# Kernel optimization log

Measured on AMD Instinct MI355X. Metric: run time of the kernel, lower is better.

Reference implementation:

```python
import jax, jax.numpy as jnp
import numpy as np

N_NODES = 65536
N_EDGES = 1048576
D = 128           # input_dim == hidden_dim*heads, residual active everywhere
HEADS = (4, 4, 1) # heads per GATv2 layer; last layer heads=1, out=input_dim
NUM_LAYERS = 3


def setup_inputs() -> dict:
    key = jax.random.key(0)
    ks = jax.random.split(key, 16)
    x = jax.random.normal(ks[0], (N_NODES, D), dtype=jnp.float32)
    edge_src = jax.random.randint(ks[1], (N_EDGES,), 0, N_NODES)
    edge_dst = jax.random.randint(ks[2], (N_EDGES,), 0, N_NODES)
    edge_attr = jax.random.uniform(ks[3], (N_EDGES, 1), dtype=jnp.float32)
    s = 0.05
    Wl = jax.random.normal(ks[4], (NUM_LAYERS, D, D), dtype=jnp.float32) * s
    bl = jnp.zeros((NUM_LAYERS, D), dtype=jnp.float32)
    Wr = jax.random.normal(ks[5], (NUM_LAYERS, D, D), dtype=jnp.float32) * s
    br = jnp.zeros((NUM_LAYERS, D), dtype=jnp.float32)
    We = jax.random.normal(ks[6], (NUM_LAYERS, 1, D), dtype=jnp.float32) * s
    att = jax.random.normal(ks[7], (NUM_LAYERS, D), dtype=jnp.float32) * s  # reshaped (H,C) per layer
    bias_p = jnp.zeros((NUM_LAYERS, D), dtype=jnp.float32)
    ln_g = jnp.ones((NUM_LAYERS, D), dtype=jnp.float32)
    ln_b = jnp.zeros((NUM_LAYERS, D), dtype=jnp.float32)
    return {"x": x, "edge_src": edge_src, "edge_dst": edge_dst, "edge_attr": edge_attr,
            "Wl": Wl, "bl": bl, "Wr": Wr, "br": br, "We": We, "att": att,
            "bias_p": bias_p, "ln_g": ln_g, "ln_b": ln_b, "num_graphs": 128}


def _layer_norm(x, g, b):
    mu = x.mean(-1, keepdims=True)
    var = jnp.mean((x - mu) ** 2, axis=-1, keepdims=True)
    return (x - mu) * jax.lax.rsqrt(var + 1e-5) * g + b


def _gatv2(x, src, dst, ea, Wl, bl, Wr, br, We, att, bias, H):
    # GATv2Conv, eval mode (no dropout), concat heads
    N = x.shape[0]
    HC = Wl.shape[1]
    C = HC // H
    xl = (x @ Wl + bl).reshape(N, H, C)
    xr = (x @ Wr + br).reshape(N, H, C)
    ee = (ea @ We).reshape(-1, H, C)            # [E, H, C]
    m = xl[src] + xr[dst] + ee                  # gather + fuse edge features
    m = jnp.where(m >= 0, m, 0.2 * m)           # leaky_relu(0.2)
    a = jnp.einsum('ehc,hc->eh', m, att.reshape(H, C))
    # scatter-softmax over destination node neighborhoods
    amax = jax.ops.segment_max(a, dst, num_segments=N)
    ae = jnp.exp(a - amax[dst])
    asum = jax.ops.segment_sum(ae, dst, num_segments=N)
    alpha = ae / (asum[dst] + 1e-16)
    out = jax.ops.segment_sum(xl[src] * alpha[:, :, None], dst, num_segments=N)
    return out.reshape(N, HC) + bias


def reference(x, edge_src, edge_dst, edge_attr, Wl, bl, Wr, br, We, att,
              bias_p, ln_g, ln_b, num_graphs):
    N = x.shape[0]
    # add_self_loops=True with fill_value='mean' for edge_attr (PyG default)
    loop = jnp.arange(N, dtype=edge_src.dtype)
    src = jnp.concatenate([edge_src, loop])
    dst = jnp.concatenate([edge_dst, loop])
    ea_mean = edge_attr.mean(0, keepdims=True)
    ea = jnp.concatenate([edge_attr, jnp.broadcast_to(ea_mean, (N, edge_attr.shape[1]))])
    h = x
    for i in range(NUM_LAYERS):
        out = _gatv2(h, src, dst, ea, Wl[i], bl[i], Wr[i], br[i], We[i],
                     att[i], bias_p[i], HEADS[i])
        out = _layer_norm(out, ln_g[i], ln_b[i])
        if i < NUM_LAYERS - 1:
            out = jax.nn.gelu(out, approximate=False)
        h = h + out  # residual: dims match at every layer by construction
    # to_dense_batch with equal-size graphs, then drop virtual node (last per graph)
    x_dense = h.reshape(num_graphs, -1, h.shape[-1])
    return x_dense[:, :-1, :]
```

## Files before the change

### kernel.cpp

```cpp
#include <hip/hip_runtime.h>
#include <hip/hip_bf16.h>

typedef unsigned int uint;
typedef unsigned short ushort;

#define NN 65536
#define NE 1048576
#define DD 128
#define TOTE (NE + NN)

__device__ __forceinline__ float b2f(ushort u) {
    uint v = ((uint)u) << 16; float f; __builtin_memcpy(&f, &v, 4); return f;
}
__device__ __forceinline__ ushort f2b(float f) {
    uint x; __builtin_memcpy(&x, &f, 4);
    uint r = (x + 0x7fffu + ((x >> 16) & 1u)) >> 16;
    return (ushort)r;
}

typedef __bf16 bf16x8 __attribute__((ext_vector_type(8)));
typedef float f32x4 __attribute__((ext_vector_type(4)));
typedef float f32x2 __attribute__((ext_vector_type(2)));

__device__ __forceinline__ f32x2 bf2f2(uint u) {
    union { uint i; float f; } lo, hi;
    lo.i = u << 16; hi.i = u & 0xffff0000u;
    return (f32x2){lo.f, hi.f};
}


__global__ void k_init(const float* __restrict__ Wl, const float* __restrict__ Wr,
                       ushort* __restrict__ WT, int* __restrict__ cnt, float* __restrict__ sumbuf,
                       float* __restrict__ cano) {
    if (cano && blockIdx.x == 0 && blockIdx.y == 0 && blockIdx.z == 0 && threadIdx.x == 0)
        cano[0] = 100.0f;
    int k = blockIdx.x, n = threadIdx.x, lr = blockIdx.y, layer = blockIdx.z;
    const float* W = (lr ? Wr : Wl) + layer * 16384;
    WT[(layer * 2 + lr) * 16384 + n * 128 + k] = f2b(W[k * 128 + n]);
    int gid = ((blockIdx.z * 2 + blockIdx.y) * 128 + blockIdx.x) * 128 + threadIdx.x;
    if (gid < NN) cnt[gid] = 0;
    if (gid == NN) sumbuf[0] = 0.f;
}

__global__ void k_histsum(const int* __restrict__ dst, const float* __restrict__ ea,
                          int* __restrict__ cnt, float* __restrict__ sum,
                          float* __restrict__ cano) {
    if (cano && blockIdx.x == 0 && threadIdx.x == 0) cano[1] = 120.0f;
    __shared__ float red[256];
    int t = threadIdx.x;
    int e0 = (blockIdx.x * 256 + t) * 4;
    float s = 0.f;
    if (e0 < NE) {
        int4  d4 = *(const int4*)&dst[e0];
        float4 a4 = *(const float4*)&ea[e0];
        atomicAdd(&cnt[d4.x], 1); atomicAdd(&cnt[d4.y], 1);
        atomicAdd(&cnt[d4.z], 1); atomicAdd(&cnt[d4.w], 1);
        s = (a4.x + a4.y) + (a4.z + a4.w);
    } else {
        int b = e0 - NE;
        atomicAdd(&cnt[b], 1);     atomicAdd(&cnt[b + 1], 1);
        atomicAdd(&cnt[b + 2], 1); atomicAdd(&cnt[b + 3], 1);
    }
    red[t] = s; __syncthreads();
    for (int o = 128; o > 0; o >>= 1) { if (t < o) red[t] += red[t + o]; __syncthreads(); }
    if (t == 0 && red[0] != 0.f) atomicAdd(sum, red[0]);
}

__global__ void k_scanA(const int* __restrict__ cnt, int* __restrict__ row_off, int* __restrict__ bsum,
                        float* __restrict__ cano) {
    if (cano && blockIdx.x == 0 && threadIdx.x == 0) cano[2] = 140.0f;
    __shared__ int tmp[256];
    int t = threadIdx.x, i = blockIdx.x * 256 + t;
    int v = cnt[i]; tmp[t] = v; __syncthreads();
    for (int off = 1; off < 256; off <<= 1) {
        int x = (t >= off) ? tmp[t - off] : 0;
        __syncthreads();
        tmp[t] += x;
        __syncthreads();
    }
    row_off[i] = tmp[t] - v;
    if (t == 255) bsum[blockIdx.x] = tmp[255];
}

__global__ void k_scanC(int* __restrict__ row_off, const int* __restrict__ bsum, int* __restrict__ cursor,
                        float* __restrict__ cano) {
    if (cano && blockIdx.x == 0 && threadIdx.x == 0) cano[3] = 160.0f;
    __shared__ int tmp[256];
    __shared__ int excl[256];
    int t = threadIdx.x;
    int v = bsum[t]; tmp[t] = v; __syncthreads();
    for (int off = 1; off < 256; off <<= 1) {
        int x = (t >= off) ? tmp[t - off] : 0;
        __syncthreads();
        tmp[t] += x;
        __syncthreads();
    }
    excl[t] = tmp[t] - v;
    __syncthreads();
    int offb = excl[blockIdx.x];
    int i = blockIdx.x * 256 + t;
    int nv = row_off[i] + offb;
    row_off[i] = nv;
    cursor[i] = nv;
    if (i == 0) row_off[NN] = TOTE;
}

__global__ void k_scatter(const int* __restrict__ src, const int* __restrict__ dst,
                          const float* __restrict__ ea, const float* __restrict__ sum,
                          int* __restrict__ cursor, int2* __restrict__ adj,
                          float* __restrict__ cano) {
    if (cano && blockIdx.x == 0 && threadIdx.x == 0) cano[4] = 180.0f;
    int e0 = (blockIdx.x * 256 + threadIdx.x) * 4;
    if (e0 < NE) {
        int4  s4 = *(const int4*)&src[e0];
        int4  d4 = *(const int4*)&dst[e0];
        float4 a4 = *(const float4*)&ea[e0];
        int p0 = atomicAdd(&cursor[d4.x], 1); adj[p0] = make_int2(s4.x << 8, __float_as_int(a4.x));
        int p1 = atomicAdd(&cursor[d4.y], 1); adj[p1] = make_int2(s4.y << 8, __float_as_int(a4.y));
        int p2 = atomicAdd(&cursor[d4.z], 1); adj[p2] = make_int2(s4.z << 8, __float_as_int(a4.z));
        int p3 = atomicAdd(&cursor[d4.w], 1); adj[p3] = make_int2(s4.w << 8, __float_as_int(a4.w));
    } else {
        int b = e0 - NE;
        float a = sum[0] * (1.0f / NE);
        #pragma unroll
        for (int k = 0; k < 4; k++) {
            int p = atomicAdd(&cursor[b + k], 1);
            adj[p] = make_int2((b + k) << 8, __float_as_int(a));
        }
    }
}

template<bool F32SRC>
__global__ __launch_bounds__(512) void k_gemm(const void* __restrict__ srcv, const ushort* __restrict__ WT,
                                              const float* __restrict__ bl, const float* __restrict__ br,
                                              ushort* __restrict__ xl, ushort* __restrict__ xr,
                                              float* __restrict__ cano, int cslot, float cval) {
    if (cano && blockIdx.x == 0 && threadIdx.x == 0) cano[cslot] = cval;
    __shared__ __align__(16) ushort S[32768];

    int t = threadIdx.x;
    int rowbase = blockIdx.x * 128;

    #pragma unroll
    for (int i = 0; i < 8; i++) {
        int idx = i * 512 + t;
        int m = idx >> 11, n = (idx >> 4) & 127, c = idx & 15;
        *(bf16x8*)&S[m * 16384 + c * 1024 + n * 8] =
            *(const bf16x8*)&WT[m * 16384 + n * 128 + c * 8];
    }

    int wave = t >> 6, lane = t & 63;
    int row16 = lane & 15, quad = lane >> 4;
    int myrow = rowbase + wave * 16 + row16;

    bf16x8 areg[4];
    if (F32SRC) {
        const float* src = (const float*)srcv;
        float4 av[8];
        #pragma unroll
        for (int ks = 0; ks < 4; ks++) {
            const float* pa = &src[(size_t)myrow * 128 + ks * 32 + quad * 8];
            av[2 * ks]     = *(const float4*)pa;
            av[2 * ks + 1] = *(const float4*)(pa + 4);
        }
        #pragma unroll
        for (int ks = 0; ks < 4; ks++) {
            ushort u[8] = {f2b(av[2 * ks].x), f2b(av[2 * ks].y), f2b(av[2 * ks].z), f2b(av[2 * ks].w),
                           f2b(av[2 * ks + 1].x), f2b(av[2 * ks + 1].y), f2b(av[2 * ks + 1].z), f2b(av[2 * ks + 1].w)};
            __builtin_memcpy(&areg[ks], u, 16);
        }
    } else {
        const ushort* src = (const ushort*)srcv;
        #pragma unroll
        for (int ks = 0; ks < 4; ks++)
            areg[ks] = *(const bf16x8*)&src[(size_t)myrow * 128 + ks * 32 + quad * 8];
    }

    float bbl[8], bbr[8];
    #pragma unroll
    for (int tc = 0; tc < 8; tc++) { bbl[tc] = bl[tc * 16 + row16]; bbr[tc] = br[tc * 16 + row16]; }

    f32x4 accl[8], accr[8];
    #pragma unroll
    for (int i = 0; i < 8; i++) {
        accl[i] = (f32x4){0.f, 0.f, 0.f, 0.f};
        accr[i] = (f32x4){0.f, 0.f, 0.f, 0.f};
    }

    __syncthreads();

    #pragma unroll
    for (int ks = 0; ks < 4; ks++) {
        int chunk = ks * 4 + quad;
        #pragma unroll
        for (int tc = 0; tc < 8; tc++) {
            int coln = tc * 16 + row16;
            bf16x8 b_l = *(const bf16x8*)&S[chunk * 1024 + coln * 8];
            bf16x8 b_r = *(const bf16x8*)&S[16384 + chunk * 1024 + coln * 8];
            accl[tc] = __builtin_amdgcn_mfma_f32_16x16x32_bf16(areg[ks], b_l, accl[tc], 0, 0, 0);
            accr[tc] = __builtin_amdgcn_mfma_f32_16x16x32_bf16(areg[ks], b_r, accr[tc], 0, 0, 0);
        }
    }

    __syncthreads();

    #pragma unroll
    for (int tc = 0; tc < 8; tc++) {
        int col = tc * 16 + row16;
        #pragma unroll
        for (int r = 0; r < 4; r++) {
            int row = wave * 16 + quad * 4 + r;
            S[row * 128 + col]         = f2b(accl[tc][r] + bbl[tc]);
            S[16384 + row * 128 + col] = f2b(accr[tc][r] + bbr[tc]);
        }
    }
    __syncthreads();

    #pragma unroll
    for (int i = 0; i < 8; i++) {
        int idx = i * 512 + t;
        int m = idx >> 11, row = (idx >> 4) & 127, c8 = idx & 15;
        bf16x8 v = *(const bf16x8*)&S[m * 16384 + row * 128 + c8 * 8];
        ushort* dst = m ? xr : xl;
        *(bf16x8*)&dst[(size_t)(rowbase + row) * 128 + c8 * 8] = v;
    }
}

template<int H, bool FINAL>
__global__ __launch_bounds__(128, 4) void k_attn(
    const ushort* __restrict__ xl, const ushort* __restrict__ xr,
    const int* __restrict__ row_off, const int2* __restrict__ adj,
    const float* __restrict__ We, const float* __restrict__ att,
    const float* __restrict__ bias, const float* __restrict__ ln_g, const float* __restrict__ ln_b,
    const float* __restrict__ hin, float* __restrict__ hout, ushort* __restrict__ hb,
    float* __restrict__ outp,
    float* __restrict__ cano, int cslot, float cval)
{
    if (cano && blockIdx.x == 0 && threadIdx.x == 0) cano[cslot] = cval;
    __shared__ float accbuf[2][8][160];

    int wv = threadIdx.x >> 6, lane = threadIdx.x & 63;
    int n = blockIdx.x * 2 + wv;
    int p = lane >> 3;
    int cl = lane & 7;
    int c16 = cl * 16;
    const char* xlb = (const char*)xl;

    f32x2 we2[8], at2[8], xrl2[8];
    #pragma unroll
    for (int k = 0; k < 8; k++) {
        we2[k] = (f32x2){We[c16 + 2 * k], We[c16 + 2 * k + 1]};
        at2[k] = (f32x2){att[c16 + 2 * k], att[c16 + 2 * k + 1]};
    }
    {
        uint4 r0 = *(const uint4*)&xr[(size_t)n * 128 + c16];
        uint4 r1 = *(const uint4*)&xr[(size_t)n * 128 + c16 + 8];
        xrl2[0] = bf2f2(r0.x); xrl2[1] = bf2f2(r0.y); xrl2[2] = bf2f2(r0.z); xrl2[3] = bf2f2(r0.w);
        xrl2[4] = bf2f2(r1.x); xrl2[5] = bf2f2(r1.y); xrl2[6] = bf2f2(r1.z); xrl2[7] = bf2f2(r1.w);
    }

    int s0 = row_off[n], s1 = row_off[n + 1];
    int iters = (s1 - s0 + 7) >> 3;

    float l_run = 0.f;
    f32x2 acc[8];
    #pragma unroll
    for (int k = 0; k < 8; k++) acc[k] = (f32x2){0.f, 0.f};

    int j0 = s0 + p,      j1 = s0 + 8 + p,  j2 = s0 + 16 + p, j3 = s0 + 24 + p;
    int i0 = (j0 < s1) ? j0 : s0;
    int i1 = (j1 < s1) ? j1 : s0;
    int i2 = (j2 < s1) ? j2 : s0;
    int i3 = (j3 < s1) ? j3 : s0;
    int2 a0 = adj[i0], a1 = adj[i1], a2 = adj[i2], a3 = adj[i3];
    float ea0 = (j0 < s1) ? __int_as_float(a0.y) : 0.f;
    float ea1 = (j1 < s1) ? __int_as_float(a1.y) : 0.f;
    float ea2v = (j2 < s1) ? __int_as_float(a2.y) : 0.f;
    float ea3 = (j3 < s1) ? __int_as_float(a3.y) : 0.f;
    const char* q0 = xlb + (size_t)(uint)a0.x + (cl << 5);
    const char* q1 = xlb + (size_t)(uint)a1.x + (cl << 5);
    const char* q2 = xlb + (size_t)(uint)a2.x + (cl << 5);
    const char* q3 = xlb + (size_t)(uint)a3.x + (cl << 5);
    uint4 u00 = *(const uint4*)q0, u01 = *(const uint4*)(q0 + 16);
    uint4 u10 = *(const uint4*)q1, u11 = *(const uint4*)(q1 + 16);
    uint4 u20 = *(const uint4*)q2, u21 = *(const uint4*)(q2 + 16);
    uint4 u30 = *(const uint4*)q3, u31 = *(const uint4*)(q3 + 16);

    auto consume = [&](uint4 u0, uint4 u1, float ea_c, int itx) {
        bool valid = (s0 + itx * 8 + p) < s1;
        f32x2 xf[8];
        xf[0] = bf2f2(u0.x); xf[1] = bf2f2(u0.y); xf[2] = bf2f2(u0.z); xf[3] = bf2f2(u0.w);
        xf[4] = bf2f2(u1.x); xf[5] = bf2f2(u1.y); xf[6] = bf2f2(u1.z); xf[7] = bf2f2(u1.w);

        f32x2 ea2 = (f32x2){ea_c, ea_c};
        f32x2 s2 = (f32x2){0.f, 0.f};
        #pragma unroll
        for (int k = 0; k < 8; k++) {
            f32x2 m = xf[k] + __builtin_elementwise_fma(ea2, we2[k], xrl2[k]);
            m = __builtin_elementwise_max(m, 0.2f * m);
            s2 = __builtin_elementwise_fma(m, at2[k], s2);
        }
        float s = s2.x + s2.y;
        s += __shfl_xor(s, 1);
        if (H == 1) { s += __shfl_xor(s, 2); s += __shfl_xor(s, 4); }
        if (!valid) s = -1e30f;

        float e = __expf(s);
        l_run += e;
        f32x2 e2 = (f32x2){e, e};
        #pragma unroll
        for (int k = 0; k < 8; k++) acc[k] = __builtin_elementwise_fma(e2, xf[k], acc[k]);
    };

    consume(u00, u01, ea0, 0);
    if (iters > 1) consume(u10, u11, ea1, 1);
    if (iters > 2) consume(u20, u21, ea2v, 2);
    if (iters > 3) consume(u30, u31, ea3, 3);
    for (int it = 4; it < iters; ++it) {
        int jn = s0 + it * 8 + p;
        int jb = (jn < s1) ? jn : s0;
        int2 pk = adj[jb];
        float ean = (jn < s1) ? __int_as_float(pk.y) : 0.f;
        const char* rp = xlb + (size_t)(uint)pk.x + (cl << 5);
        uint4 nu0 = *(const uint4*)rp;
        uint4 nu1 = *(const uint4*)(rp + 16);
        consume(nu0, nu1, ean, it);
    }

    l_run += __shfl_xor(l_run, 8);
    l_run += __shfl_xor(l_run, 16);
    l_run += __shfl_xor(l_run, 32);
    float inv = 1.0f / (l_run + 1e-16f);

    float* row = &accbuf[wv][p][cl * 20];
    #pragma unroll
    for (int i = 0; i < 4; i++)
        *(float4*)&row[4 * i] = make_float4(acc[2 * i].x * inv, acc[2 * i].y * inv,
                                            acc[2 * i + 1].x * inv, acc[2 * i + 1].y * inv);
    __syncthreads();

    int c0 = 2 * lane;
    int rb = (c0 >> 4) * 20 + (c0 & 15);
    float o0 = 0.f, o1 = 0.f;
    #pragma unroll
    for (int q = 0; q < 8; q++) {
        float2 v = *(float2*)&accbuf[wv][q][rb];
        o0 += v.x; o1 += v.y;
    }
    o0 += bias[c0];
    o1 += bias[c0 + 1];

    float sred = o0 + o1;
    #pragma unroll
    for (int off = 1; off < 64; off <<= 1) sred += __shfl_xor(sred, off);
    float mu = sred * (1.f / 128.f);
    float d0 = o0 - mu, d1 = o1 - mu;
    float v = d0 * d0 + d1 * d1;
    #pragma unroll
    for (int off = 1; off < 64; off <<= 1) v += __shfl_xor(v, off);
    float rstd = rsqrtf(v * (1.f / 128.f) + 1e-5f);
    o0 = d0 * rstd * ln_g[c0] + ln_b[c0];
    o1 = d1 * rstd * ln_g[c0 + 1] + ln_b[c0 + 1];

    float2 hv = *(const float2*)&hin[(size_t)n * 128 + c0];
    if (FINAL) {
        float r0 = hv.x + o0, r1 = hv.y + o1;
        int g = n >> 9, rr = n & 511;
        if (rr < 511)
            *(float2*)&outp[((size_t)(g * 511 + rr)) * 128 + c0] = make_float2(r0, r1);
    } else {
        float t0 = o0 * (0.79788456f + 0.03567741f * o0 * o0);
        o0 = __fdividef(o0, 1.f + __expf(-2.f * t0));
        float t1 = o1 * (0.79788456f + 0.03567741f * o1 * o1);
        o1 = __fdividef(o1, 1.f + __expf(-2.f * t1));
        hv.x += o0; hv.y += o1;
        *(float2*)&hout[(size_t)n * 128 + c0] = hv;
        uint pk = (uint)f2b(hv.x) | ((uint)f2b(hv.y) << 16);
        *(uint*)&hb[(size_t)n * 128 + c0] = pk;
    }
}

extern "C" void kernel_launch(void* const* d_in, const int* in_sizes, int n_in,
                              void* d_out, int out_size, void* d_ws, size_t ws_size,
                              hipStream_t stream) {
    const float* x        = (const float*)d_in[0];
    const int*   edge_src = (const int*)d_in[1];
    const int*   edge_dst = (const int*)d_in[2];
    const float* edge_attr= (const float*)d_in[3];
    const float* Wl       = (const float*)d_in[4];
    const float* bl       = (const float*)d_in[5];
    const float* Wr       = (const float*)d_in[6];
    const float* br       = (const float*)d_in[7];
    const float* We       = (const float*)d_in[8];
    const float* att      = (const float*)d_in[9];
    const float* bias_p   = (const float*)d_in[10];
    const float* ln_g     = (const float*)d_in[11];
    const float* ln_b     = (const float*)d_in[12];
    float* out = (float*)d_out;

    char* ws = (char*)d_ws;
    float*  h       = (float*)(ws + 0);
    ushort* hb      = (ushort*)(ws + 33554432);
    ushort* xl      = (ushort*)(ws + 50331648);
    ushort* xr      = (ushort*)(ws + 67108864);
    int2*   adj     = (int2*)(ws + 83886080);
    int*    row_off = (int*)(ws + 92798976);
    int*    cnt     = (int*)(ws + 93061376);
    int*    bsum    = (int*)(ws + 93323520);
    float*  sumbuf  = (float*)(ws + 93324544);
    ushort* WT      = (ushort*)(ws + 93324800);

    k_init<<<dim3(128, 2, 3), 128, 0, stream>>>(Wl, Wr, WT, cnt, sumbuf, out);
    k_histsum<<<TOTE / 1024, 256, 0, stream>>>(edge_dst, edge_attr, cnt, sumbuf, out);
    k_scanA<<<NN / 256, 256, 0, stream>>>(cnt, row_off, bsum, out);
    k_scanC<<<NN / 256, 256, 0, stream>>>(row_off, bsum, cnt, out);
    k_scatter<<<TOTE / 1024, 256, 0, stream>>>(edge_src, edge_dst, edge_attr, sumbuf, cnt, adj, out);

    k_gemm<true><<<NN / 128, 512, 0, stream>>>(x, WT, bl, br, xl, xr, out, 5, 200.0f);
    k_attn<4, false><<<NN / 2, 128, 0, stream>>>(xl, xr, row_off, adj,
                                                 We, att, bias_p, ln_g, ln_b,
                                                 x, h, hb, nullptr, out, 6, 220.0f);
    k_gemm<false><<<NN / 128, 512, 0, stream>>>(hb, WT + 32768, bl + 128, br + 128, xl, xr, out, 7, 240.0f);
    k_attn<4, false><<<NN / 2, 128, 0, stream>>>(xl, xr, row_off, adj,
                                                 We + 128, att + 128, bias_p + 128,
                                                 ln_g + 128, ln_b + 128,
                                                 h, h, hb, nullptr, out, 8, 260.0f);
    k_gemm<false><<<NN / 128, 512, 0, stream>>>(hb, WT + 65536, bl + 256, br + 256, xl, xr, out, 9, 280.0f);
    k_attn<1, true><<<NN / 2, 128, 0, stream>>>(xl, xr, row_off, adj,
                                                We + 256, att + 256, bias_p + 256,
                                                ln_g + 256, ln_b + 256,
                                                h, nullptr, nullptr, out, nullptr, 0, 0.0f);
}
```

Measured before the change: 520.9 us.

## Process two destination nodes per wave in attention kernel with overlapped prefetch

Each wave now handles two consecutive destination nodes. It issues the xr loads, adjacency loads and first four neighbor-row gathers for both nodes up front, then consumes them in turn. This is meant to expose more memory-level parallelism and hide gather latency. In exchange it raises register pressure (launch bounds lowered to 2), halves the grid, and adds an extra block barrier per epilogue.

```diff
diff --git a/kernel.cpp b/kernel.cpp
--- a/kernel.cpp
+++ b/kernel.cpp
@@ -227,7 +227,7 @@
 }
 
 template<int H, bool FINAL>
-__global__ __launch_bounds__(128, 4) void k_attn(
+__global__ __launch_bounds__(128, 2) void k_attn(
     const ushort* __restrict__ xl, const ushort* __restrict__ xr,
     const int* __restrict__ row_off, const int2* __restrict__ adj,
     const float* __restrict__ We, const float* __restrict__ att,
@@ -240,63 +240,76 @@
     __shared__ float accbuf[2][8][160];
 
     int wv = threadIdx.x >> 6, lane = threadIdx.x & 63;
-    int n = blockIdx.x * 2 + wv;
     int p = lane >> 3;
     int cl = lane & 7;
     int c16 = cl * 16;
     const char* xlb = (const char*)xl;
 
-    f32x2 we2[8], at2[8], xrl2[8];
+    f32x2 we2[8], at2[8];
     #pragma unroll
     for (int k = 0; k < 8; k++) {
         we2[k] = (f32x2){We[c16 + 2 * k], We[c16 + 2 * k + 1]};
         at2[k] = (f32x2){att[c16 + 2 * k], att[c16 + 2 * k + 1]};
     }
-    {
-        uint4 r0 = *(const uint4*)&xr[(size_t)n * 128 + c16];
-        uint4 r1 = *(const uint4*)&xr[(size_t)n * 128 + c16 + 8];
-        xrl2[0] = bf2f2(r0.x); xrl2[1] = bf2f2(r0.y); xrl2[2] = bf2f2(r0.z); xrl2[3] = bf2f2(r0.w);
-        xrl2[4] = bf2f2(r1.x); xrl2[5] = bf2f2(r1.y); xrl2[6] = bf2f2(r1.z); xrl2[7] = bf2f2(r1.w);
-    }
-
-    int s0 = row_off[n], s1 = row_off[n + 1];
-    int iters = (s1 - s0 + 7) >> 3;
-
-    float l_run = 0.f;
-    f32x2 acc[8];
-    #pragma unroll
-    for (int k = 0; k < 8; k++) acc[k] = (f32x2){0.f, 0.f};
-
-    int j0 = s0 + p,      j1 = s0 + 8 + p,  j2 = s0 + 16 + p, j3 = s0 + 24 + p;
-    int i0 = (j0 < s1) ? j0 : s0;
-    int i1 = (j1 < s1) ? j1 : s0;
-    int i2 = (j2 < s1) ? j2 : s0;
-    int i3 = (j3 < s1) ? j3 : s0;
-    int2 a0 = adj[i0], a1 = adj[i1], a2 = adj[i2], a3 = adj[i3];
-    float ea0 = (j0 < s1) ? __int_as_float(a0.y) : 0.f;
-    float ea1 = (j1 < s1) ? __int_as_float(a1.y) : 0.f;
-    float ea2v = (j2 < s1) ? __int_as_float(a2.y) : 0.f;
-    float ea3 = (j3 < s1) ? __int_as_float(a3.y) : 0.f;
-    const char* q0 = xlb + (size_t)(uint)a0.x + (cl << 5);
-    const char* q1 = xlb + (size_t)(uint)a1.x + (cl << 5);
-    const char* q2 = xlb + (size_t)(uint)a2.x + (cl << 5);
-    const char* q3 = xlb + (size_t)(uint)a3.x + (cl << 5);
-    uint4 u00 = *(const uint4*)q0, u01 = *(const uint4*)(q0 + 16);
-    uint4 u10 = *(const uint4*)q1, u11 = *(const uint4*)(q1 + 16);
-    uint4 u20 = *(const uint4*)q2, u21 = *(const uint4*)(q2 + 16);
-    uint4 u30 = *(const uint4*)q3, u31 = *(const uint4*)(q3 + 16);
-
-    auto consume = [&](uint4 u0, uint4 u1, float ea_c, int itx) {
-        bool valid = (s0 + itx * 8 + p) < s1;
+    int c0 = 2 * lane;
+    int rb = (c0 >> 4) * 20 + (c0 & 15);
+
+    int nA = blockIdx.x * 4 + wv * 2;
+    int nB = nA + 1;
+    int s0a = row_off[nA];
+    int s1a = row_off[nA + 1];
+    int s1b = row_off[nA + 2];
+    int s0b = s1a;
+
+    uint4 xra0 = *(const uint4*)&xr[(size_t)nA * 128 + c16];
+    uint4 xra1 = *(const uint4*)&xr[(size_t)nA * 128 + c16 + 8];
+    uint4 xrb0 = *(const uint4*)&xr[(size_t)nB * 128 + c16];
+    uint4 xrb1 = *(const uint4*)&xr[(size_t)nB * 128 + c16 + 8];
+
+    int jA0 = s0a + p, jA1 = s0a + 8 + p, jA2 = s0a + 16 + p, jA3 = s0a + 24 + p;
+    int2 aA0 = adj[(jA0 < s1a) ? jA0 : s0a];
+    int2 aA1 = adj[(jA1 < s1a) ? jA1 : s0a];
+    int2 aA2 = adj[(jA2 < s1a) ? jA2 : s0a];
+    int2 aA3 = adj[(jA3 < s1a) ? jA3 : s0a];
+    int jB0 = s0b + p, jB1 = s0b + 8 + p, jB2 = s0b + 16 + p, jB3 = s0b + 24 + p;
+    int2 aB0 = adj[(jB0 < s1b) ? jB0 : s0b];
+    int2 aB1 = adj[(jB1 < s1b) ? jB1 : s0b];
+    int2 aB2 = adj[(jB2 < s1b) ? jB2 : s0b];
+    int2 aB3 = adj[(jB3 < s1b) ? jB3 : s0b];
+
+    const char* qA0 = xlb + (size_t)(uint)aA0.x + (cl << 5);
+    const char* qA1 = xlb + (size_t)(uint)aA1.x + (cl << 5);
+    const char* qA2 = xlb + (size_t)(uint)aA2.x + (cl << 5);
+    const char* qA3 = xlb + (size_t)(uint)aA3.x + (cl << 5);
+    uint4 uA00 = *(const uint4*)qA0, uA01 = *(const uint4*)(qA0 + 16);
+    uint4 uA10 = *(const uint4*)qA1, uA11 = *(const uint4*)(qA1 + 16);
+    uint4 uA20 = *(const uint4*)qA2, uA21 = *(const uint4*)(qA2 + 16);
+    uint4 uA30 = *(const uint4*)qA3, uA31 = *(const uint4*)(qA3 + 16);
+    const char* qB0 = xlb + (size_t)(uint)aB0.x + (cl << 5);
+    const char* qB1 = xlb + (size_t)(uint)aB1.x + (cl << 5);
+    const char* qB2 = xlb + (size_t)(uint)aB2.x + (cl << 5);
+    const char* qB3 = xlb + (size_t)(uint)aB3.x + (cl << 5);
+    uint4 uB00 = *(const uint4*)qB0, uB01 = *(const uint4*)(qB0 + 16);
+    uint4 uB10 = *(const uint4*)qB1, uB11 = *(const uint4*)(qB1 + 16);
+    uint4 uB20 = *(const uint4*)qB2, uB21 = *(const uint4*)(qB2 + 16);
+    uint4 uB30 = *(const uint4*)qB3, uB31 = *(const uint4*)(qB3 + 16);
+
+    f32x2 xrlA[8], xrlB[8];
+    xrlA[0] = bf2f2(xra0.x); xrlA[1] = bf2f2(xra0.y); xrlA[2] = bf2f2(xra0.z); xrlA[3] = bf2f2(xra0.w);
+    xrlA[4] = bf2f2(xra1.x); xrlA[5] = bf2f2(xra1.y); xrlA[6] = bf2f2(xra1.z); xrlA[7] = bf2f2(xra1.w);
+    xrlB[0] = bf2f2(xrb0.x); xrlB[1] = bf2f2(xrb0.y); xrlB[2] = bf2f2(xrb0.z); xrlB[3] = bf2f2(xrb0.w);
+    xrlB[4] = bf2f2(xrb1.x); xrlB[5] = bf2f2(xrb1.y); xrlB[6] = bf2f2(xrb1.z); xrlB[7] = bf2f2(xrb1.w);
+
+    auto consume = [&](uint4 u0, uint4 u1, float ea_c, bool valid,
+                       const f32x2* xrl, float& lr, f32x2* ac) {
         f32x2 xf[8];
         xf[0] = bf2f2(u0.x); xf[1] = bf2f2(u0.y); xf[2] = bf2f2(u0.z); xf[3] = bf2f2(u0.w);
         xf[4] = bf2f2(u1.x); xf[5] = bf2f2(u1.y); xf[6] = bf2f2(u1.z); xf[7] = bf2f2(u1.w);
-
         f32x2 ea2 = (f32x2){ea_c, ea_c};
         f32x2 s2 = (f32x2){0.f, 0.f};
         #pragma unroll
         for (int k = 0; k < 8; k++) {
-            f32x2 m = xf[k] + __builtin_elementwise_fma(ea2, we2[k], xrl2[k]);
+            f32x2 m = xf[k] + __builtin_elementwise_fma(ea2, we2[k], xrl[k]);
             m = __builtin_elementwise_max(m, 0.2f * m);
             s2 = __builtin_elementwise_fma(m, at2[k], s2);
         }
@@ -304,80 +317,106 @@
         s += __shfl_xor(s, 1);
         if (H == 1) { s += __shfl_xor(s, 2); s += __shfl_xor(s, 4); }
         if (!valid) s = -1e30f;
-
         float e = __expf(s);
-        l_run += e;
+        lr += e;
         f32x2 e2 = (f32x2){e, e};
         #pragma unroll
-        for (int k = 0; k < 8; k++) acc[k] = __builtin_elementwise_fma(e2, xf[k], acc[k]);
+        for (int k = 0; k < 8; k++) ac[k] = __builtin_elementwise_fma(e2, xf[k], ac[k]);
     };
 
-    consume(u00, u01, ea0, 0);
-    if (iters > 1) consume(u10, u11, ea1, 1);
-    if (iters > 2) consume(u20, u21, ea2v, 2);
-    if (iters > 3) consume(u30, u31, ea3, 3);
-    for (int it = 4; it < iters; ++it) {
-        int jn = s0 + it * 8 + p;
-        int jb = (jn < s1) ? jn : s0;
+    int itersA = (s1a - s0a + 7) >> 3;
+    float lA = 0.f;
+    f32x2 accA[8];
+    #pragma unroll
+    for (int k = 0; k < 8; k++) accA[k] = (f32x2){0.f, 0.f};
+    consume(uA00, uA01, (jA0 < s1a) ? __int_as_float(aA0.y) : 0.f, jA0 < s1a, xrlA, lA, accA);
+    if (itersA > 1) consume(uA10, uA11, (jA1 < s1a) ? __int_as_float(aA1.y) : 0.f, jA1 < s1a, xrlA, lA, accA);
+    if (itersA > 2) consume(uA20, uA21, (jA2 < s1a) ? __int_as_float(aA2.y) : 0.f, jA2 < s1a, xrlA, lA, accA);
+    if (itersA > 3) consume(uA30, uA31, (jA3 < s1a) ? __int_as_float(aA3.y) : 0.f, jA3 < s1a, xrlA, lA, accA);
+    for (int it = 4; it < itersA; ++it) {
+        int jn = s0a + it * 8 + p;
+        int jb = (jn < s1a) ? jn : s0a;
         int2 pk = adj[jb];
-        float ean = (jn < s1) ? __int_as_float(pk.y) : 0.f;
         const char* rp = xlb + (size_t)(uint)pk.x + (cl << 5);
         uint4 nu0 = *(const uint4*)rp;
         uint4 nu1 = *(const uint4*)(rp + 16);
-        consume(nu0, nu1, ean, it);
-    }
-
-    l_run += __shfl_xor(l_run, 8);
-    l_run += __shfl_xor(l_run, 16);
-    l_run += __shfl_xor(l_run, 32);
-    float inv = 1.0f / (l_run + 1e-16f);
-
-    float* row = &accbuf[wv][p][cl * 20];
-    #pragma unroll
-    for (int i = 0; i < 4; i++)
-        *(float4*)&row[4 * i] = make_float4(acc[2 * i].x * inv, acc[2 * i].y * inv,
-                                            acc[2 * i + 1].x * inv, acc[2 * i + 1].y * inv);
-    __syncthreads();
-
-    int c0 = 2 * lane;
-    int rb = (c0 >> 4) * 20 + (c0 & 15);
-    float o0 = 0.f, o1 = 0.f;
-    #pragma unroll
-    for (int q = 0; q < 8; q++) {
-        float2 v = *(float2*)&accbuf[wv][q][rb];
-        o0 += v.x; o1 += v.y;
-    }
-    o0 += bias[c0];
-    o1 += bias[c0 + 1];
-
-    float sred = o0 + o1;
-    #pragma unroll
-    for (int off = 1; off < 64; off <<= 1) sred += __shfl_xor(sred, off);
-    float mu = sred * (1.f / 128.f);
-    float d0 = o0 - mu, d1 = o1 - mu;
-    float v = d0 * d0 + d1 * d1;
-    #pragma unroll
-    for (int off = 1; off < 64; off <<= 1) v += __shfl_xor(v, off);
-    float rstd = rsqrtf(v * (1.f / 128.f) + 1e-5f);
-    o0 = d0 * rstd * ln_g[c0] + ln_b[c0];
-    o1 = d1 * rstd * ln_g[c0 + 1] + ln_b[c0 + 1];
-
-    float2 hv = *(const float2*)&hin[(size_t)n * 128 + c0];
-    if (FINAL) {
-        float r0 = hv.x + o0, r1 = hv.y + o1;
-        int g = n >> 9, rr = n & 511;
-        if (rr < 511)
-            *(float2*)&outp[((size_t)(g * 511 + rr)) * 128 + c0] = make_float2(r0, r1);
-    } else {
-        float t0 = o0 * (0.79788456f + 0.03567741f * o0 * o0);
-        o0 = __fdividef(o0, 1.f + __expf(-2.f * t0));
-        float t1 = o1 * (0.79788456f + 0.03567741f * o1 * o1);
-        o1 = __fdividef(o1, 1.f + __expf(-2.f * t1));
-        hv.x += o0; hv.y += o1;
-        *(float2*)&hout[(size_t)n * 128 + c0] = hv;
-        uint pk = (uint)f2b(hv.x) | ((uint)f2b(hv.y) << 16);
-        *(uint*)&hb[(size_t)n * 128 + c0] = pk;
-    }
+        consume(nu0, nu1, (jn < s1a) ? __int_as_float(pk.y) : 0.f, jn < s1a, xrlA, lA, accA);
+    }
+
+    int itersB = (s1b - s0b + 7) >> 3;
+    float lB = 0.f;
+    f32x2 accB[8];
+    #pragma unroll
+    for (int k = 0; k < 8; k++) accB[k] = (f32x2){0.f, 0.f};
+    consume(uB00, uB01, (jB0 < s1b) ? __int_as_float(aB0.y) : 0.f, jB0 < s1b, xrlB, lB, accB);
+    if (itersB > 1) consume(uB10, uB11, (jB1 < s1b) ? __int_as_float(aB1.y) : 0.f, jB1 < s1b, xrlB, lB, accB);
+    if (itersB > 2) consume(uB20, uB21, (jB2 < s1b) ? __int_as_float(aB2.y) : 0.f, jB2 < s1b, xrlB, lB, accB);
+    if (itersB > 3) consume(uB30, uB31, (jB3 < s1b) ? __int_as_float(aB3.y) : 0.f, jB3 < s1b, xrlB, lB, accB);
+    for (int it = 4; it < itersB; ++it) {
+        int jn = s0b + it * 8 + p;
+        int jb = (jn < s1b) ? jn : s0b;
+        int2 pk = adj[jb];
+        const char* rp = xlb + (size_t)(uint)pk.x + (cl << 5);
+        uint4 nu0 = *(const uint4*)rp;
+        uint4 nu1 = *(const uint4*)(rp + 16);
+        consume(nu0, nu1, (jn < s1b) ? __int_as_float(pk.y) : 0.f, jn < s1b, xrlB, lB, accB);
+    }
+
+    auto epilogue = [&](int n, float l_run, f32x2* acc) {
+        l_run += __shfl_xor(l_run, 8);
+        l_run += __shfl_xor(l_run, 16);
+        l_run += __shfl_xor(l_run, 32);
+        float inv = 1.0f / (l_run + 1e-16f);
+
+        float* row = &accbuf[wv][p][cl * 20];
+        #pragma unroll
+        for (int i = 0; i < 4; i++)
+            *(float4*)&row[4 * i] = make_float4(acc[2 * i].x * inv, acc[2 * i].y * inv,
+                                                acc[2 * i + 1].x * inv, acc[2 * i + 1].y * inv);
+        __syncthreads();
+
+        float o0 = 0.f, o1 = 0.f;
+        #pragma unroll
+        for (int q = 0; q < 8; q++) {
+            float2 v = *(float2*)&accbuf[wv][q][rb];
+            o0 += v.x; o1 += v.y;
+        }
+        o0 += bias[c0];
+        o1 += bias[c0 + 1];
+
+        float sred = o0 + o1;
+        #pragma unroll
+        for (int off = 1; off < 64; off <<= 1) sred += __shfl_xor(sred, off);
+        float mu = sred * (1.f / 128.f);
+        float d0 = o0 - mu, d1 = o1 - mu;
+        float v = d0 * d0 + d1 * d1;
+        #pragma unroll
+        for (int off = 1; off < 64; off <<= 1) v += __shfl_xor(v, off);
+        float rstd = rsqrtf(v * (1.f / 128.f) + 1e-5f);
+        o0 = d0 * rstd * ln_g[c0] + ln_b[c0];
+        o1 = d1 * rstd * ln_g[c0 + 1] + ln_b[c0 + 1];
+
+        float2 hv = *(const float2*)&hin[(size_t)n * 128 + c0];
+        if (FINAL) {
+            float r0 = hv.x + o0, r1 = hv.y + o1;
+            int g = n >> 9, rr = n & 511;
+            if (rr < 511)
+                *(float2*)&outp[((size_t)(g * 511 + rr)) * 128 + c0] = make_float2(r0, r1);
+        } else {
+            float t0 = o0 * (0.79788456f + 0.03567741f * o0 * o0);
+            o0 = __fdividef(o0, 1.f + __expf(-2.f * t0));
+            float t1 = o1 * (0.79788456f + 0.03567741f * o1 * o1);
+            o1 = __fdividef(o1, 1.f + __expf(-2.f * t1));
+            hv.x += o0; hv.y += o1;
+            *(float2*)&hout[(size_t)n * 128 + c0] = hv;
+            uint pk = (uint)f2b(hv.x) | ((uint)f2b(hv.y) << 16);
+            *(uint*)&hb[(size_t)n * 128 + c0] = pk;
+        }
+        __syncthreads();
+    };
+
+    epilogue(nA, lA, accA);
+    epilogue(nB, lB, accB);
 }
 
 extern "C" void kernel_launch(void* const* d_in, const int* in_sizes, int n_in,
@@ -417,16 +456,16 @@
     k_scatter<<<TOTE / 1024, 256, 0, stream>>>(edge_src, edge_dst, edge_attr, sumbuf, cnt, adj, out);
 
     k_gemm<true><<<NN / 128, 512, 0, stream>>>(x, WT, bl, br, xl, xr, out, 5, 200.0f);
-    k_attn<4, false><<<NN / 2, 128, 0, stream>>>(xl, xr, row_off, adj,
+    k_attn<4, false><<<NN / 4, 128, 0, stream>>>(xl, xr, row_off, adj,
                                                  We, att, bias_p, ln_g, ln_b,
                                                  x, h, hb, nullptr, out, 6, 220.0f);
     k_gemm<false><<<NN / 128, 512, 0, stream>>>(hb, WT + 32768, bl + 128, br + 128, xl, xr, out, 7, 240.0f);
-    k_attn<4, false><<<NN / 2, 128, 0, stream>>>(xl, xr, row_off, adj,
+    k_attn<4, false><<<NN / 4, 128, 0, stream>>>(xl, xr, row_off, adj,
                                                  We + 128, att + 128, bias_p + 128,
                                                  ln_g + 128, ln_b + 128,
                                                  h, h, hb, nullptr, out, 8, 260.0f);
     k_gemm<false><<<NN / 128, 512, 0, stream>>>(hb, WT + 65536, bl + 256, br + 256, xl, xr, out, 9, 280.0f);
-    k_attn<1, true><<<NN / 2, 128, 0, stream>>>(xl, xr, row_off, adj,
+    k_attn<1, true><<<NN / 4, 128, 0, stream>>>(xl, xr, row_off, adj,
                                                 We + 256, att + 256, bias_p + 256,
                                                 ln_g + 256, ln_b + 256,
                                                 h, nullptr, nullptr, out, nullptr, 0, 0.0f);
```

After: 571.8 us. +9.8%, slower.
